# Kernel optimization log

Measured on AMD Instinct MI355X. Metric: run time of the kernel, lower is better.

The kernel has to match this reference:

```python
import jax, jax.numpy as jnp
import numpy as np

B, T, IN, H, Z, DH, K = 512, 256, 5, 256, 128, 512, 20
OUT = 6 * K + 3


def setup_inputs() -> dict:
    key = jax.random.key(0)
    ks = jax.random.split(key, 24)
    p = lambda k, shp: jax.random.normal(k, shp, dtype=jnp.float32) * 0.05
    return {
        "s": jax.random.normal(ks[0], (B, T, IN), dtype=jnp.float32),
        "epsilon": jax.random.normal(ks[1], (Z,), dtype=jnp.float32),
        "Wih_f": p(ks[2], (4 * H, IN)), "Whh_f": p(ks[3], (4 * H, H)),
        "bih_f": p(ks[4], (4 * H,)), "bhh_f": p(ks[5], (4 * H,)),
        "Wih_b": p(ks[6], (4 * H, IN)), "Whh_b": p(ks[7], (4 * H, H)),
        "bih_b": p(ks[8], (4 * H,)), "bhh_b": p(ks[9], (4 * H,)),
        "W_sigma": p(ks[10], (Z, 2 * H)), "b_sigma": p(ks[11], (Z,)),
        "W_mu": p(ks[12], (Z, 2 * H)), "b_mu": p(ks[13], (Z,)),
        "W_h0": p(ks[14], (DH, Z)), "b_h0": p(ks[15], (DH,)),
        "Wih_d": p(ks[16], (4 * DH, IN + Z)), "Whh_d": p(ks[17], (4 * DH, DH)),
        "bih_d": p(ks[18], (4 * DH,)), "bhh_d": p(ks[19], (4 * DH,)),
        "W_dec": p(ks[20], (OUT, DH)), "b_dec": p(ks[21], (OUT,)),
    }


def _lstm_scan(x, Wih, Whh, b, reverse):
    # x: [T, B, in]; PyTorch gate order i, f, g, o
    Hh = Whh.shape[1]
    h0 = jnp.zeros((x.shape[1], Hh), x.dtype)

    def step(carry, xt):
        h, c = carry
        g = xt @ Wih.T + h @ Whh.T + b
        i, f, gg, o = jnp.split(g, 4, axis=-1)
        c = jax.nn.sigmoid(f) * c + jax.nn.sigmoid(i) * jnp.tanh(gg)
        h = jax.nn.sigmoid(o) * jnp.tanh(c)
        return (h, c), h

    _, hs = jax.lax.scan(step, (h0, h0), x, reverse=reverse)
    return hs  # [T, B, Hh]


def _mdn(y):
    # y: [..., 123] -> per-mixture (pi, mu1, mu2, sx, sy, corr) + 3 pen logits
    mix = y[..., :6 * K].reshape(y.shape[:-1] + (K, 6))
    pi = jax.nn.softmax(mix[..., 0], axis=-1)
    out_mix = jnp.stack(
        [pi, mix[..., 1], mix[..., 2], jnp.exp(mix[..., 3]),
         jnp.exp(mix[..., 4]), jnp.tanh(mix[..., 5])], axis=-1)
    pen = jax.nn.softmax(y[..., 6 * K:], axis=-1)
    return jnp.concatenate([out_mix.reshape(y.shape[:-1] + (6 * K,)), pen], axis=-1)


def reference(s, epsilon, Wih_f, Whh_f, bih_f, bhh_f, Wih_b, Whh_b, bih_b, bhh_b,
              W_sigma, b_sigma, W_mu, b_mu, W_h0, b_h0,
              Wih_d, Whh_d, bih_d, bhh_d, W_dec, b_dec):
    x = jnp.transpose(s, (1, 0, 2))  # [T, B, 5]
    hf = _lstm_scan(x, Wih_f, Whh_f, bih_f + bhh_f, False)
    hb = _lstm_scan(x, Wih_b, Whh_b, bih_b + bhh_b, True)
    h = jnp.concatenate([hf[-1], hb[-1]], axis=-1)  # output at last time step, [B, 512]
    presig = h @ W_sigma.T + b_sigma
    mu = h @ W_mu.T + b_mu
    sigma = jnp.exp(presig / 2)
    z = mu + sigma * epsilon  # [B, Z]
    h0 = jnp.tanh(z @ W_h0.T + b_h0)
    c0 = jnp.zeros((s.shape[0], DH), s.dtype)
    s0 = jnp.tile(jnp.array([0.0, 0.0, 1.0, 0.0, 0.0], s.dtype), (s.shape[0], 1))
    dec_in = jnp.concatenate([s0[None], x[:T - 1]], axis=0)  # [T, B, 5]
    bdec = bih_d + bhh_d

    def step(carry, st):
        hh, cc = carry
        xt = jnp.concatenate([st, z], axis=-1)  # [B, 133]
        g = xt @ Wih_d.T + hh @ Whh_d.T + bdec
        i, f, gg, o = jnp.split(g, 4, axis=-1)
        cc = jax.nn.sigmoid(f) * cc + jax.nn.sigmoid(i) * jnp.tanh(gg)
        hh = jax.nn.sigmoid(o) * jnp.tanh(cc)
        y = hh @ W_dec.T + b_dec
        return (hh, cc), y

    _, ys = jax.lax.scan(step, (h0, c0), dec_in)  # [T, B, 123]
    output = _mdn(jnp.transpose(ys, (1, 0, 2)))   # [B, T, 123]
    return (output, mu, presig)
```

## Files before the change

kernel.cpp:

```cpp
#include <hip/hip_runtime.h>

typedef unsigned short u16;
typedef unsigned long long u64;
typedef __attribute__((ext_vector_type(8))) short bfrag;
typedef __attribute__((ext_vector_type(4))) float f32x4;

#define MFMA __builtin_amdgcn_mfma_f32_16x16x32_bf16

#define OFF_FLAGS 0ull
#define OFF_HENC  4096ull
#define OFF_WENC  528384ull
#define OFF_WDEC  1118208ull
#define OFF_WY    3870720ull
#define OFF_WMS   4001792ull
#define OFF_WH0   4280320ull
#define OFF_HDEC  4444160ull
#define OFF_HLAT  5492736ull
#define OFF_AZ    6049792ull
#define OFF_SX    6213632ull

__device__ __forceinline__ u16 f2bf(float f) {
  union { float f; unsigned int i; } v; v.f = f;
  unsigned int r = v.i + 0x7fffu + ((v.i >> 16) & 1u);
  return (u16)(r >> 16);
}
__device__ __forceinline__ float sigm(float x) { return 1.0f / (1.0f + __expf(-x)); }
__device__ __forceinline__ float tanh_(float x) {
  float a = fabsf(x);
  float e = __expf(-2.0f * a);
  float r = (1.0f - e) / (1.0f + e);
  return x < 0.0f ? -r : r;
}

__device__ __forceinline__ u64 aload(const u64* p) {
  return __hip_atomic_load(p, __ATOMIC_RELAXED, __HIP_MEMORY_SCOPE_AGENT);
}
__device__ __forceinline__ void astore(u64* p, u64 v) {
  __hip_atomic_store(p, v, __ATOMIC_RELAXED, __HIP_MEMORY_SCOPE_AGENT);
}
__device__ __forceinline__ float afload(const float* p) {
  return __hip_atomic_load(p, __ATOMIC_RELAXED, __HIP_MEMORY_SCOPE_AGENT);
}
__device__ __forceinline__ void afstore(float* p, float v) {
  __hip_atomic_store(p, v, __ATOMIC_RELAXED, __HIP_MEMORY_SCOPE_AGENT);
}

__device__ __forceinline__ void gwait(int* base, int ep, int tid, int* sdead) {
  if (ep > 0) {
    if (tid < 32 && *sdead == 0) {
      int* fp = base + tid;
      int spin = 0;
      while (__hip_atomic_load(fp, __ATOMIC_RELAXED, __HIP_MEMORY_SCOPE_AGENT) < ep) {
        __builtin_amdgcn_s_sleep(1);
        if (++spin > (1 << 18)) { *sdead = 1; break; }
      }
    }
  }
  __syncthreads();
  asm volatile("" ::: "memory");
}
__device__ __forceinline__ void garrive(int* base, int m, int ep, int tid) {
  asm volatile("s_waitcnt vmcnt(0)" ::: "memory");
  __syncthreads();
  if (tid == 0)
    __hip_atomic_store(base + m, ep, __ATOMIC_RELAXED, __HIP_MEMORY_SCOPE_AGENT);
}

__global__ void pack_wenc(const float* __restrict__ Whh, const float* __restrict__ Wih,
                          const float* __restrict__ bi, const float* __restrict__ bh,
                          u16* __restrict__ out) {
  int idx = blockIdx.x * 256 + threadIdx.x;
  if (idx >= 294912) return;
  int m = idx / 9216, within = idx % 9216;
  int kb = within >> 10, rest = within & 1023;
  int ng = rest >> 9, l = (rest >> 3) & 63, j = rest & 7;
  int nl = ng * 16 + (l & 15);
  int u = nl >> 2, g = nl & 3;
  int row = g * 256 + m * 8 + u;
  int k = kb * 32 + (l >> 4) * 8 + j;
  float v = 0.f;
  if (k < 256) v = Whh[row * 256 + k];
  else if (k < 261) v = Wih[row * 5 + (k - 256)];
  else if (k == 261) v = bi[row] + bh[row];
  out[idx] = f2bf(v);
}

__global__ void pack_wdec(const float* __restrict__ Whh, const float* __restrict__ Wih,
                          const float* __restrict__ bi, const float* __restrict__ bh,
                          u16* __restrict__ out) {
  int idx = blockIdx.x * 256 + threadIdx.x;
  if (idx >= 1376256) return;
  int m = idx / 43008, within = idx % 43008;
  int kb = within >> 11, rest = within & 2047;
  int w = rest >> 9, l = (rest >> 3) & 63, j = rest & 7;
  int nl = w * 16 + (l & 15);
  int u = nl >> 2, g = nl & 3;
  int row = g * 512 + m * 16 + u;
  int k = kb * 32 + (l >> 4) * 8 + j;
  float v = 0.f;
  if (k < 512) v = Whh[row * 512 + k];
  else if (k < 640) v = Wih[row * 133 + 5 + (k - 512)];
  else if (k < 645) v = Wih[row * 133 + (k - 640)];
  else if (k == 645) v = bi[row] + bh[row];
  out[idx] = f2bf(v);
}

__global__ void pack_wy(const float* __restrict__ Wd, u16* __restrict__ out) {
  int idx = blockIdx.x * 256 + threadIdx.x;
  if (idx >= 65536) return;
  int m = idx >> 13, within = idx & 8191;
  int kb = within >> 9, rest = within & 511;
  int l = rest >> 3, j = rest & 7;
  int row = m * 16 + (l & 15);
  int k = kb * 32 + (l >> 4) * 8 + j;
  float v = (row < 123 && k < 512) ? Wd[row * 512 + k] : 0.f;
  out[idx] = f2bf(v);
}

__global__ void pack_wms(const float* __restrict__ Wmu, const float* __restrict__ bmu,
                         const float* __restrict__ Wsig, const float* __restrict__ bsig,
                         u16* __restrict__ out) {
  int idx = blockIdx.x * 256 + threadIdx.x;
  if (idx >= 139264) return;
  int r = idx / 544, k = idx % 544;
  float v = 0.f;
  if (r < 128) {
    if (k < 512) v = Wmu[r * 512 + k];
    else if (k == 512) v = bmu[r];
  } else {
    int r2 = r - 128;
    if (k < 512) v = Wsig[r2 * 512 + k];
    else if (k == 512) v = bsig[r2];
  }
  out[idx] = f2bf(v);
}

__global__ void pack_wh0(const float* __restrict__ Wh0, const float* __restrict__ bh0,
                         u16* __restrict__ out) {
  int idx = blockIdx.x * 256 + threadIdx.x;
  if (idx >= 81920) return;
  int r = idx / 160, k = idx % 160;
  float v = 0.f;
  if (k < 128) v = Wh0[r * 128 + k];
  else if (k == 128) v = bh0[r];
  out[idx] = f2bf(v);
}

__global__ void pack_sx(const float* __restrict__ s, u16* __restrict__ out) {
  int idx = blockIdx.x * 256 + threadIdx.x;
  if (idx >= 1048576) return;
  int j = idx & 7, b = (idx >> 3) & 511, t = idx >> 12;
  u16 v;
  if (j < 5) v = f2bf(s[((size_t)b * 256 + t) * 5 + j]);
  else v = (j == 5) ? (u16)0x3F80 : (u16)0;
  out[idx] = v;
}

__global__ __launch_bounds__(256, 1) void rnn_persist(
    int* __restrict__ flags, u16* __restrict__ henc,
    const u16* __restrict__ WENCP, const u16* __restrict__ WDECP,
    const u16* __restrict__ WYP, const u16* __restrict__ WMSP, const u16* __restrict__ WH0P,
    u16* __restrict__ hdec, u16* __restrict__ hlat, u16* __restrict__ Az,
    const u16* __restrict__ SXD,
    const float* __restrict__ s, const float* __restrict__ eps,
    const float* __restrict__ Wih_b, const float* __restrict__ bih_b,
    const float* __restrict__ bhh_b,
    const float* __restrict__ b_dec, float* __restrict__ out)
{
  __shared__ __align__(16) u16 sm[72960];
  __shared__ __align__(16) float gbuf[2112];
  __shared__ __align__(16) u16 hst[1024];
  __shared__ int sdead;

  const int tid = threadIdx.x;
  const int blk = blockIdx.x;
  const int g = blk & 7;
  const int m = blk >> 3;
  const int B0 = g * 64;
  const int w = tid >> 6, l = tid & 63;
  const int lr = l & 15, ko = (l >> 4) * 8;
  int* FA = flags + g * 128;
  int* FB = FA + 64;

  float* out_mu = out + 16121856;
  float* out_ps = out + 16187392;

  const int gcol = m * 16 + lr;
  float bd = 0.f;
  if (m < 8 && gcol < 123) bd = b_dec[gcol];

  if (tid == 0) sdead = 0;
  {
    bfrag zz = {0, 0, 0, 0, 0, 0, 0, 0};
    #pragma unroll
    for (int i = 0; i < 5; ++i) {
      int c = i * 256 + tid;
      if (c < 1184) *(bfrag*)(sm + c * 8) = zz;
    }
  }
  {
    const u16* src = WENCP + (size_t)m * 9216;
    #pragma unroll
    for (int i = 0; i < 5; ++i) {
      int c = i * 256 + tid;
      if (c < 1152) *(bfrag*)(sm + 21760 + c * 8) = *(const bfrag*)(src + c * 8);
    }
  }
  __syncthreads();

  float c_enc0 = 0.f, c_enc1 = 0.f;
  #pragma unroll 1
  for (int t = 0; t < 256; ++t) {
    #pragma unroll
    for (int X = 0; X < 2; ++X) {
      int* F = X ? FB : FA;
      gwait(F, t, tid, &sdead);
      const u64* hs = (const u64*)(henc + (size_t)((t + 1) & 1) * 131072 +
                                   (size_t)(B0 + X * 32) * 256);
      u64 hv[8];
      #pragma unroll
      for (int i = 0; i < 8; ++i) hv[i] = aload(hs + i * 256 + tid);
      #pragma unroll
      for (int i = 0; i < 8; ++i) {
        int idx = i * 256 + tid;
        *(u64*)(sm + (idx >> 6) * 296 + (idx & 63) * 4) = hv[i];
      }
      if (tid < 64) {
        int row = tid >> 1, q = tid & 1;
        *(u64*)(sm + row * 296 + 256 + q * 4) =
            *(const u64*)(SXD + ((size_t)(t * 512 + B0 + X * 32 + row)) * 8 + q * 4);
      }
      __syncthreads();
      const int mt = w >> 1, ng = w & 1;
      f32x4 acc = {0.f, 0.f, 0.f, 0.f};
      #pragma unroll
      for (int kb = 0; kb < 9; ++kb) {
        bfrag a = *(const bfrag*)(sm + (mt * 16 + lr) * 296 + kb * 32 + ko);
        bfrag bw = *(const bfrag*)(sm + 21760 + (kb * 2 + ng) * 512 + l * 8);
        acc = MFMA(a, bw, acc, 0, 0, 0);
      }
      #pragma unroll
      for (int j = 0; j < 4; ++j)
        gbuf[(mt * 16 + (l >> 4) * 4 + j) * 33 + ng * 16 + lr] = acc[j];
      __syncthreads();
      {
        int bl = tid >> 3, u = tid & 7;
        float gi = gbuf[bl * 33 + u * 4 + 0], gf = gbuf[bl * 33 + u * 4 + 1];
        float gg = gbuf[bl * 33 + u * 4 + 2], go = gbuf[bl * 33 + u * 4 + 3];
        float cprev = (X == 0) ? c_enc0 : c_enc1;
        float c = sigm(gf) * cprev + sigm(gi) * tanh_(gg);
        if (X == 0) c_enc0 = c; else c_enc1 = c;
        hst[bl * 8 + u] = f2bf(sigm(go) * tanh_(c));
      }
      __syncthreads();
      if (tid < 64) {
        int row = tid >> 1, q = tid & 1;
        u64 v = *(const u64*)(hst + row * 8 + q * 4);
        astore((u64*)(henc + (size_t)(t & 1) * 131072 +
                      (size_t)(B0 + X * 32 + row) * 256 + m * 8) + q, v);
      }
      garrive(F, m, t + 1, tid);
    }
  }

  u16* lat_hf = (u16*)gbuf;
  u16* lat_hb = (u16*)gbuf + 512;
  u16* lat_z  = (u16*)gbuf + 1024;

  gwait(FA, 256, tid, &sdead);
  gwait(FB, 256, tid, &sdead);
  {
    const u16* src = WDECP + (size_t)m * 43008;
    #pragma unroll 1
    for (int i = 0; i < 21; ++i) {
      int c = i * 256 + tid;
      *(bfrag*)(sm + 21760 + c * 8) = *(const bfrag*)(src + c * 8);
    }
  }
  if (m < 8) {
    const u16* src = WYP + (size_t)m * 8192;
    #pragma unroll
    for (int i = 0; i < 4; ++i) {
      int c = i * 256 + tid;
      *(bfrag*)(sm + 64768 + c * 8) = *(const bfrag*)(src + c * 8);
    }
  }
  #pragma unroll
  for (int r = 0; r < 2; ++r) {
    int b = B0 + m * 2 + r;
    if (tid < 64) {
      u64 v = aload((const u64*)(henc + 131072 + (size_t)b * 256) + tid);
      *(u64*)(lat_hf + r * 256 + tid * 4) = v;
    }
    {
      const float* xr = s + ((size_t)b * 256 + 255) * 5;
      float x0 = xr[0], x1 = xr[1], x2 = xr[2], x3 = xr[3], x4 = xr[4];
      int n = tid;
      float gv[4];
      #pragma unroll
      for (int gg = 0; gg < 4; ++gg) {
        int row = gg * 256 + n;
        gv[gg] = bih_b[row] + bhh_b[row] + x0 * Wih_b[row * 5] + x1 * Wih_b[row * 5 + 1] +
                 x2 * Wih_b[row * 5 + 2] + x3 * Wih_b[row * 5 + 3] + x4 * Wih_b[row * 5 + 4];
      }
      float c = sigm(gv[0]) * tanh_(gv[2]);
      lat_hb[r * 256 + n] = f2bf(sigm(gv[3]) * tanh_(c));
    }
  }
  __syncthreads();
  #pragma unroll
  for (int it = 0; it < 2; ++it) {
    int idx = it * 256 + tid;
    if (idx < 272) {
      int rr = idx / 136, u = idx % 136;
      u64 pv = 0;
      #pragma unroll
      for (int q = 0; q < 4; ++q) {
        int c = u * 4 + q;
        u16 x;
        if (c < 256) x = lat_hf[rr * 256 + c];
        else if (c < 512) x = lat_hb[rr * 256 + c - 256];
        else if (c == 512) x = 0x3F80;
        else x = 0;
        pv |= ((u64)x) << (q * 16);
      }
      astore((u64*)(hlat + (size_t)(B0 + m * 2 + rr) * 544) + u, pv);
    }
  }
  garrive(FA, m, 257, tid);

  gwait(FA, 257, tid, &sdead);
  {
    const int bH = m >> 4, cT = m & 15;
    const u64* src = (const u64*)(hlat + (size_t)(B0 + bH * 32) * 544);
    u64 sv[17];
    #pragma unroll
    for (int i = 0; i < 17; ++i) sv[i] = aload(src + i * 256 + tid);
    #pragma unroll
    for (int i = 0; i < 17; ++i) *(u64*)(sm + (i * 256 + tid) * 4) = sv[i];
    __syncthreads();
    if (w < 2) {
      f32x4 acc = {0.f, 0.f, 0.f, 0.f};
      const u16* bp = WMSP + (size_t)(cT * 16 + lr) * 544 + ko;
      #pragma unroll
      for (int kb = 0; kb < 17; ++kb) {
        bfrag a = *(const bfrag*)(sm + (w * 16 + lr) * 544 + kb * 32 + ko);
        bfrag bb = *(const bfrag*)(bp + kb * 32);
        acc = MFMA(a, bb, acc, 0, 0, 0);
      }
      int nc = cT * 16 + lr;
      #pragma unroll
      for (int j = 0; j < 4; ++j) {
        int b = B0 + bH * 32 + w * 16 + (l >> 4) * 4 + j;
        if (nc < 128) afstore(out_mu + (size_t)b * 128 + nc, acc[j]);
        else afstore(out_ps + (size_t)b * 128 + nc - 128, acc[j]);
      }
    }
  }
  garrive(FA, m, 258, tid);

  gwait(FA, 258, tid, &sdead);
  {
    int r = tid >> 7, zj = tid & 127;
    int b = B0 + m * 2 + r;
    float mu = afload(out_mu + (size_t)b * 128 + zj);
    float ps = afload(out_ps + (size_t)b * 128 + zj);
    float z = mu + __expf(0.5f * ps) * eps[zj];
    lat_z[r * 128 + zj] = f2bf(z);
  }
  __syncthreads();
  if (tid < 80) {
    int r = tid / 40, u = tid % 40;
    u64 pv = 0;
    #pragma unroll
    for (int q = 0; q < 4; ++q) {
      int c = u * 4 + q;
      u16 x;
      if (c < 128) x = lat_z[r * 128 + c];
      else if (c == 128) x = 0x3F80;
      else x = 0;
      pv |= ((u64)x) << (q * 16);
    }
    astore((u64*)(Az + (size_t)(B0 + m * 2 + r) * 160) + u, pv);
  }
  garrive(FA, m, 259, tid);

  gwait(FA, 259, tid, &sdead);
  u64 zreg0[4], zreg1[4];
  {
    int r = tid >> 3;
    #pragma unroll
    for (int i = 0; i < 4; ++i) {
      int uu = (tid & 7) * 4 + i;
      zreg0[i] = aload((const u64*)(Az + (size_t)(B0 + r) * 160) + uu);
      zreg1[i] = aload((const u64*)(Az + (size_t)(B0 + 32 + r) * 160) + uu);
    }
  }
  {
    const u64* src = (const u64*)(Az + (size_t)B0 * 160);
    u64 sv[10];
    #pragma unroll
    for (int i = 0; i < 10; ++i) sv[i] = aload(src + i * 256 + tid);
    #pragma unroll
    for (int i = 0; i < 10; ++i) *(u64*)(sm + (i * 256 + tid) * 4) = sv[i];
    __syncthreads();
    f32x4 acc = {0.f, 0.f, 0.f, 0.f};
    const u16* bp = WH0P + (size_t)(m * 16 + lr) * 160 + ko;
    #pragma unroll
    for (int kb = 0; kb < 5; ++kb) {
      bfrag a = *(const bfrag*)(sm + (w * 16 + lr) * 160 + kb * 32 + ko);
      bfrag bb = *(const bfrag*)(bp + kb * 32);
      acc = MFMA(a, bb, acc, 0, 0, 0);
    }
    #pragma unroll
    for (int j = 0; j < 4; ++j)
      hst[(w * 16 + (l >> 4) * 4 + j) * 16 + lr] = f2bf(tanh_(acc[j]));
  }
  __syncthreads();
  #pragma unroll
  for (int i = 0; i < 5; ++i) {
    int idx = i * 256 + tid;
    if (idx < 1120) {
      int row = idx / 35, c = idx % 35;
      sm[row * 680 + 645 + c] = (c == 0) ? 0x3F80 : 0;
    }
  }
  {
    int row = tid >> 2, q = tid & 3;
    u64 v = *(const u64*)(hst + row * 16 + q * 4);
    astore((u64*)(hdec + 262144 + (size_t)(B0 + row) * 512 + m * 16) + q, v);
  }
  garrive(FA, m, 260, tid);
  if (tid == 0)
    __hip_atomic_store(FB + m, 257, __ATOMIC_RELAXED, __HIP_MEMORY_SCOPE_AGENT);

  float c_dec00 = 0.f, c_dec01 = 0.f, c_dec10 = 0.f, c_dec11 = 0.f;
  #pragma unroll 1
  for (int t = 0; t < 256; ++t) {
    #pragma unroll
    for (int X = 0; X < 2; ++X) {
      int* F = X ? FB : FA;
      int base = X ? 257 : 260;
      gwait(F, base + t, tid, &sdead);
      const u64* hs = (const u64*)(hdec + (size_t)((t + 1) & 1) * 262144 +
                                   (size_t)(B0 + X * 32) * 512);
      u64 hv[16];
      #pragma unroll
      for (int i = 0; i < 16; ++i) hv[i] = aload(hs + i * 256 + tid);
      #pragma unroll
      for (int i = 0; i < 16; ++i) {
        int idx = i * 256 + tid;
        *(u64*)(sm + (idx >> 7) * 680 + (idx & 127) * 4) = hv[i];
      }
      {
        int r = tid >> 3;
        #pragma unroll
        for (int i = 0; i < 4; ++i) {
          int uu = (tid & 7) * 4 + i;
          *(u64*)(sm + r * 680 + 512 + uu * 4) = (X == 0) ? zreg0[i] : zreg1[i];
        }
      }
      if (tid < 64) {
        int row = tid >> 1, q = tid & 1;
        u64 v;
        if (t == 0) v = q ? 0x000000003F800000ULL : 0x00003F8000000000ULL;
        else v = *(const u64*)(SXD + ((size_t)((t - 1) * 512 + B0 + X * 32 + row)) * 8 + q * 4);
        *(u64*)(sm + row * 680 + 640 + q * 4) = v;
      }
      __syncthreads();
      const int mtd = w & 1, nb = (w >> 1) * 2;
      const bool doy = (m < 8) && (w < 2) && (t > 0);
      f32x4 acc0 = {0.f, 0.f, 0.f, 0.f}, acc1 = {0.f, 0.f, 0.f, 0.f}, accy = {0.f, 0.f, 0.f, 0.f};
      #pragma unroll
      for (int kb = 0; kb < 21; ++kb) {
        bfrag a  = *(const bfrag*)(sm + (mtd * 16 + lr) * 680 + kb * 32 + ko);
        bfrag b0 = *(const bfrag*)(sm + 21760 + kb * 2048 + nb * 512 + l * 8);
        bfrag b1 = *(const bfrag*)(sm + 21760 + kb * 2048 + (nb + 1) * 512 + l * 8);
        acc0 = MFMA(a, b0, acc0, 0, 0, 0);
        acc1 = MFMA(a, b1, acc1, 0, 0, 0);
        if (kb < 16 && doy) {
          bfrag by = *(const bfrag*)(sm + 64768 + kb * 512 + l * 8);
          accy = MFMA(a, by, accy, 0, 0, 0);
        }
      }
      if (doy && gcol < 123) {
        int brow = B0 + X * 32 + w * 16 + (l >> 4) * 4;
        #pragma unroll
        for (int j = 0; j < 4; ++j)
          out[((size_t)(brow + j) * 256 + (t - 1)) * 123 + gcol] = accy[j] + bd;
      }
      #pragma unroll
      for (int j = 0; j < 4; ++j) {
        int grow = mtd * 16 + (l >> 4) * 4 + j;
        gbuf[grow * 66 + nb * 16 + lr] = acc0[j];
        gbuf[grow * 66 + (nb + 1) * 16 + lr] = acc1[j];
      }
      __syncthreads();
      #pragma unroll
      for (int p = 0; p < 2; ++p) {
        int idx = p * 256 + tid;
        int bl = idx >> 4, u = idx & 15;
        float gi = gbuf[bl * 66 + u * 4 + 0], gf = gbuf[bl * 66 + u * 4 + 1];
        float gg = gbuf[bl * 66 + u * 4 + 2], go = gbuf[bl * 66 + u * 4 + 3];
        float cprev = (X == 0) ? (p == 0 ? c_dec00 : c_dec01) : (p == 0 ? c_dec10 : c_dec11);
        float c = sigm(gf) * cprev + sigm(gi) * tanh_(gg);
        if (X == 0) { if (p == 0) c_dec00 = c; else c_dec01 = c; }
        else        { if (p == 0) c_dec10 = c; else c_dec11 = c; }
        hst[bl * 16 + u] = f2bf(sigm(go) * tanh_(c));
      }
      __syncthreads();
      if (tid < 128) {
        int row = tid >> 2, q = tid & 3;
        u64 v = *(const u64*)(hst + row * 16 + q * 4);
        astore((u64*)(hdec + (size_t)(t & 1) * 262144 +
                      (size_t)(B0 + X * 32 + row) * 512 + m * 16) + q, v);
      }
      garrive(F, m, base + t + 1, tid);
    }
  }

  gwait(FA, 516, tid, &sdead);
  gwait(FB, 513, tid, &sdead);
  #pragma unroll
  for (int X = 0; X < 2; ++X) {
    const u64* hsrc = (const u64*)(hdec + 262144 + (size_t)(B0 + X * 32) * 512);
    u64 hv[16];
    #pragma unroll
    for (int i = 0; i < 16; ++i) hv[i] = aload(hsrc + i * 256 + tid);
    #pragma unroll
    for (int i = 0; i < 16; ++i) {
      int idx = i * 256 + tid;
      *(u64*)(sm + (idx >> 7) * 680 + (idx & 127) * 4) = hv[i];
    }
    __syncthreads();
    if (m < 8 && w < 2) {
      f32x4 accy = {0.f, 0.f, 0.f, 0.f};
      #pragma unroll
      for (int kb = 0; kb < 16; ++kb) {
        bfrag a = *(const bfrag*)(sm + (w * 16 + lr) * 680 + kb * 32 + ko);
        bfrag by = *(const bfrag*)(sm + 64768 + kb * 512 + l * 8);
        accy = MFMA(a, by, accy, 0, 0, 0);
      }
      if (gcol < 123) {
        int brow = B0 + X * 32 + w * 16 + (l >> 4) * 4;
        #pragma unroll
        for (int j = 0; j < 4; ++j)
          out[((size_t)(brow + j) * 256 + 255) * 123 + gcol] = accy[j] + bd;
      }
    }
    __syncthreads();
  }
}

__global__ __launch_bounds__(64) void mdn_final(float* __restrict__ out) {
  __shared__ float rows[64 * 123];
  const int tid = threadIdx.x;
  float4* g4 = (float4*)(out + (size_t)blockIdx.x * 64 * 123);
  #pragma unroll
  for (int i = 0; i < 31; ++i) {
    int c = i * 64 + tid;
    if (c < 1968) ((float4*)rows)[c] = g4[c];
  }
  __syncthreads();
  {
    float* r = rows + tid * 123;
    float m1 = -1e30f;
    #pragma unroll
    for (int k = 0; k < 20; ++k) m1 = fmaxf(m1, r[6 * k]);
    float s1 = 0.f;
    #pragma unroll
    for (int k = 0; k < 20; ++k) s1 += __expf(r[6 * k] - m1);
    float i1 = 1.f / s1;
    #pragma unroll
    for (int k = 0; k < 20; ++k) {
      r[6 * k] = __expf(r[6 * k] - m1) * i1;
      r[6 * k + 3] = __expf(r[6 * k + 3]);
      r[6 * k + 4] = __expf(r[6 * k + 4]);
      r[6 * k + 5] = tanh_(r[6 * k + 5]);
    }
    float p0 = r[120], p1 = r[121], p2 = r[122];
    float mp = fmaxf(p0, fmaxf(p1, p2));
    float e0 = __expf(p0 - mp), e1 = __expf(p1 - mp), e2 = __expf(p2 - mp);
    float ip = 1.f / (e0 + e1 + e2);
    r[120] = e0 * ip; r[121] = e1 * ip; r[122] = e2 * ip;
  }
  __syncthreads();
  #pragma unroll
  for (int i = 0; i < 31; ++i) {
    int c = i * 64 + tid;
    if (c < 1968) g4[c] = ((float4*)rows)[c];
  }
}

extern "C" void kernel_launch(void* const* d_in, const int* in_sizes, int n_in,
                              void* d_out, int out_size, void* d_ws, size_t ws_size,
                              hipStream_t stream) {
  const float* s       = (const float*)d_in[0];
  const float* eps     = (const float*)d_in[1];
  const float* Wih_f   = (const float*)d_in[2];
  const float* Whh_f   = (const float*)d_in[3];
  const float* bih_f   = (const float*)d_in[4];
  const float* bhh_f   = (const float*)d_in[5];
  const float* Wih_b   = (const float*)d_in[6];
  const float* bih_b   = (const float*)d_in[8];
  const float* bhh_b   = (const float*)d_in[9];
  const float* W_sigma = (const float*)d_in[10];
  const float* b_sigma = (const float*)d_in[11];
  const float* W_mu    = (const float*)d_in[12];
  const float* b_mu    = (const float*)d_in[13];
  const float* W_h0    = (const float*)d_in[14];
  const float* b_h0    = (const float*)d_in[15];
  const float* Wih_d   = (const float*)d_in[16];
  const float* Whh_d   = (const float*)d_in[17];
  const float* bih_d   = (const float*)d_in[18];
  const float* bhh_d   = (const float*)d_in[19];
  const float* W_dec   = (const float*)d_in[20];
  const float* b_dec   = (const float*)d_in[21];

  char* ws = (char*)d_ws;
  int* FLAGS  = (int*)(ws + OFF_FLAGS);
  u16* HENC   = (u16*)(ws + OFF_HENC);
  u16* WENCP  = (u16*)(ws + OFF_WENC);
  u16* WDECP  = (u16*)(ws + OFF_WDEC);
  u16* WYP    = (u16*)(ws + OFF_WY);
  u16* WMSP   = (u16*)(ws + OFF_WMS);
  u16* WH0P   = (u16*)(ws + OFF_WH0);
  u16* HDEC   = (u16*)(ws + OFF_HDEC);
  u16* HLAT   = (u16*)(ws + OFF_HLAT);
  u16* AZ     = (u16*)(ws + OFF_AZ);
  u16* SXD    = (u16*)(ws + OFF_SX);
  float* out  = (float*)d_out;

  hipMemsetAsync(ws, 0, 4096 + 524288, stream);

  pack_wenc<<<1152, 256, 0, stream>>>(Whh_f, Wih_f, bih_f, bhh_f, WENCP);
  pack_wdec<<<5376, 256, 0, stream>>>(Whh_d, Wih_d, bih_d, bhh_d, WDECP);
  pack_wy<<<256, 256, 0, stream>>>(W_dec, WYP);
  pack_wms<<<544, 256, 0, stream>>>(W_mu, b_mu, W_sigma, b_sigma, WMSP);
  pack_wh0<<<320, 256, 0, stream>>>(W_h0, b_h0, WH0P);
  pack_sx<<<4096, 256, 0, stream>>>(s, SXD);

  rnn_persist<<<256, 256, 0, stream>>>(FLAGS, HENC, WENCP, WDECP, WYP, WMSP, WH0P,
                                       HDEC, HLAT, AZ, SXD, s, eps,
                                       Wih_b, bih_b, bhh_b, b_dec, out);

  mdn_final<<<2048, 64, 0, stream>>>(out);

  (void)in_sizes; (void)n_in; (void)out_size; (void)ws_size;
}
```

Measured before the change: 2.991 ms.

## Prefetch next half-batch hidden state during compute in persistent LSTM loops

The encoder and decoder recurrent loops are flattened into a single 512-iteration loop over (timestep, half-batch). Each iteration polls the flag for the next half-batch and issues its global hidden-state and input loads into registers before the current MFMA and gate work, so the load latency is hidden behind compute. The flag layout is split into separate encoder, decoder and latent-phase counters, which widens the zeroed workspace region. The decoder's constant-1 bias column now comes from the packed input rows rather than a separate LSTM pad. The extra in-flight registers (16 u64 per thread) and the more delicate cross-block ordering add register pressure and some correctness risk.

```diff
diff --git a/kernel.cpp b/kernel.cpp
--- a/kernel.cpp
+++ b/kernel.cpp
@@ -1,23 +1,26 @@
 #include <hip/hip_runtime.h>
 
 typedef unsigned short u16;
+typedef unsigned int u32;
 typedef unsigned long long u64;
 typedef __attribute__((ext_vector_type(8))) short bfrag;
 typedef __attribute__((ext_vector_type(4))) float f32x4;
 
 #define MFMA __builtin_amdgcn_mfma_f32_16x16x32_bf16
+#define VMWAIT0 asm volatile("s_waitcnt vmcnt(0)" ::: "memory")
 
 #define OFF_FLAGS 0ull
-#define OFF_HENC  4096ull
-#define OFF_WENC  528384ull
-#define OFF_WDEC  1118208ull
-#define OFF_WY    3870720ull
-#define OFF_WMS   4001792ull
-#define OFF_WH0   4280320ull
-#define OFF_HDEC  4444160ull
-#define OFF_HLAT  5492736ull
-#define OFF_AZ    6049792ull
-#define OFF_SX    6213632ull
+#define OFF_HENC  10240ull
+#define MEMSET_BYTES 534528ull
+#define OFF_WENC  534528ull
+#define OFF_WDEC  1124352ull
+#define OFF_WY    3876864ull
+#define OFF_WMS   4007936ull
+#define OFF_WH0   4286464ull
+#define OFF_HDEC  4450304ull
+#define OFF_HLAT  5498880ull
+#define OFF_AZ    6055936ull
+#define OFF_SX    6219776ull
 
 __device__ __forceinline__ u16 f2bf(float f) {
   union { float f; unsigned int i; } v; v.f = f;
@@ -45,25 +48,27 @@
   __hip_atomic_store(p, v, __ATOMIC_RELAXED, __HIP_MEMORY_SCOPE_AGENT);
 }
 
+__device__ __forceinline__ void fpoll(int* F, int need, int tid, int* sdead) {
+  if (need > 0 && tid < 32 && *sdead == 0) {
+    int spin = 0;
+    while (__hip_atomic_load(F + tid, __ATOMIC_RELAXED, __HIP_MEMORY_SCOPE_AGENT) < need) {
+      __builtin_amdgcn_s_sleep(1);
+      if (++spin > (1 << 18)) { *sdead = 1; break; }
+    }
+  }
+  asm volatile("" ::: "memory");
+}
+__device__ __forceinline__ void fset(int* F, int m, int v) {
+  __hip_atomic_store(F + m, v, __ATOMIC_RELAXED, __HIP_MEMORY_SCOPE_AGENT);
+}
 __device__ __forceinline__ void gwait(int* base, int ep, int tid, int* sdead) {
-  if (ep > 0) {
-    if (tid < 32 && *sdead == 0) {
-      int* fp = base + tid;
-      int spin = 0;
-      while (__hip_atomic_load(fp, __ATOMIC_RELAXED, __HIP_MEMORY_SCOPE_AGENT) < ep) {
-        __builtin_amdgcn_s_sleep(1);
-        if (++spin > (1 << 18)) { *sdead = 1; break; }
-      }
-    }
-  }
-  __syncthreads();
-  asm volatile("" ::: "memory");
+  fpoll(base, ep, tid, sdead);
+  __syncthreads();
 }
 __device__ __forceinline__ void garrive(int* base, int m, int ep, int tid) {
-  asm volatile("s_waitcnt vmcnt(0)" ::: "memory");
-  __syncthreads();
-  if (tid == 0)
-    __hip_atomic_store(base + m, ep, __ATOMIC_RELAXED, __HIP_MEMORY_SCOPE_AGENT);
+  VMWAIT0;
+  __syncthreads();
+  if (tid == 0) fset(base, m, ep);
 }
 
 __global__ void pack_wenc(const float* __restrict__ Whh, const float* __restrict__ Wih,
@@ -157,11 +162,10 @@
 }
 
 __global__ __launch_bounds__(256, 1) void rnn_persist(
-    int* __restrict__ flags, u16* __restrict__ henc,
+    int* __restrict__ flags, u16* __restrict__ henc, u16* __restrict__ hdec,
     const u16* __restrict__ WENCP, const u16* __restrict__ WDECP,
     const u16* __restrict__ WYP, const u16* __restrict__ WMSP, const u16* __restrict__ WH0P,
-    u16* __restrict__ hdec, u16* __restrict__ hlat, u16* __restrict__ Az,
-    const u16* __restrict__ SXD,
+    u16* __restrict__ hlat, u16* __restrict__ Az, const u16* __restrict__ SXD,
     const float* __restrict__ s, const float* __restrict__ eps,
     const float* __restrict__ Wih_b, const float* __restrict__ bih_b,
     const float* __restrict__ bhh_b,
@@ -179,8 +183,11 @@
   const int B0 = g * 64;
   const int w = tid >> 6, l = tid & 63;
   const int lr = l & 15, ko = (l >> 4) * 8;
-  int* FA = flags + g * 128;
-  int* FB = FA + 64;
+  int* FE0 = flags + g * 320;
+  int* FE1 = FE0 + 64;
+  int* FD0 = FE0 + 128;
+  int* FD1 = FE0 + 192;
+  int* FL  = FE0 + 256;
 
   float* out_mu = out + 16121856;
   float* out_ps = out + 16187392;
@@ -208,67 +215,81 @@
   }
   __syncthreads();
 
+  u64 hv[16];
+  u64 sxv = 0;
+
+  {
+    const u64* hs = (const u64*)(henc + 131072 + (size_t)B0 * 256);
+    #pragma unroll
+    for (int i = 0; i < 8; ++i) hv[i] = aload(hs + i * 256 + tid);
+    if (tid < 64)
+      sxv = *(const u64*)(SXD + (size_t)(B0 + (tid >> 1)) * 8 + (tid & 1) * 4);
+  }
   float c_enc0 = 0.f, c_enc1 = 0.f;
   #pragma unroll 1
-  for (int t = 0; t < 256; ++t) {
-    #pragma unroll
-    for (int X = 0; X < 2; ++X) {
-      int* F = X ? FB : FA;
-      gwait(F, t, tid, &sdead);
-      const u64* hs = (const u64*)(henc + (size_t)((t + 1) & 1) * 131072 +
-                                   (size_t)(B0 + X * 32) * 256);
-      u64 hv[8];
+  for (int e = 0; e < 512; ++e) {
+    const int X = e & 1, t = e >> 1;
+    VMWAIT0;
+    #pragma unroll
+    for (int i = 0; i < 8; ++i) {
+      int idx = i * 256 + tid;
+      *(u64*)(sm + (idx >> 6) * 296 + (idx & 63) * 4) = hv[i];
+    }
+    if (tid < 64) *(u64*)(sm + (tid >> 1) * 296 + 256 + (tid & 1) * 4) = sxv;
+    if (e < 511) {
+      int Xn = (e + 1) & 1, tn = (e + 1) >> 1;
+      fpoll(Xn ? FE1 : FE0, tn, tid, &sdead);
+    }
+    __syncthreads();
+    if (e < 511) {
+      int Xn = (e + 1) & 1, tn = (e + 1) >> 1;
+      const u64* hs = (const u64*)(henc + (size_t)((tn + 1) & 1) * 131072 +
+                                   (size_t)(B0 + Xn * 32) * 256);
       #pragma unroll
       for (int i = 0; i < 8; ++i) hv[i] = aload(hs + i * 256 + tid);
-      #pragma unroll
-      for (int i = 0; i < 8; ++i) {
-        int idx = i * 256 + tid;
-        *(u64*)(sm + (idx >> 6) * 296 + (idx & 63) * 4) = hv[i];
-      }
-      if (tid < 64) {
-        int row = tid >> 1, q = tid & 1;
-        *(u64*)(sm + row * 296 + 256 + q * 4) =
-            *(const u64*)(SXD + ((size_t)(t * 512 + B0 + X * 32 + row)) * 8 + q * 4);
-      }
-      __syncthreads();
-      const int mt = w >> 1, ng = w & 1;
-      f32x4 acc = {0.f, 0.f, 0.f, 0.f};
-      #pragma unroll
-      for (int kb = 0; kb < 9; ++kb) {
-        bfrag a = *(const bfrag*)(sm + (mt * 16 + lr) * 296 + kb * 32 + ko);
-        bfrag bw = *(const bfrag*)(sm + 21760 + (kb * 2 + ng) * 512 + l * 8);
-        acc = MFMA(a, bw, acc, 0, 0, 0);
-      }
-      #pragma unroll
-      for (int j = 0; j < 4; ++j)
-        gbuf[(mt * 16 + (l >> 4) * 4 + j) * 33 + ng * 16 + lr] = acc[j];
-      __syncthreads();
-      {
-        int bl = tid >> 3, u = tid & 7;
-        float gi = gbuf[bl * 33 + u * 4 + 0], gf = gbuf[bl * 33 + u * 4 + 1];
-        float gg = gbuf[bl * 33 + u * 4 + 2], go = gbuf[bl * 33 + u * 4 + 3];
-        float cprev = (X == 0) ? c_enc0 : c_enc1;
-        float c = sigm(gf) * cprev + sigm(gi) * tanh_(gg);
-        if (X == 0) c_enc0 = c; else c_enc1 = c;
-        hst[bl * 8 + u] = f2bf(sigm(go) * tanh_(c));
-      }
-      __syncthreads();
-      if (tid < 64) {
-        int row = tid >> 1, q = tid & 1;
-        u64 v = *(const u64*)(hst + row * 8 + q * 4);
-        astore((u64*)(henc + (size_t)(t & 1) * 131072 +
-                      (size_t)(B0 + X * 32 + row) * 256 + m * 8) + q, v);
-      }
-      garrive(F, m, t + 1, tid);
-    }
+      if (tid < 64)
+        sxv = *(const u64*)(SXD + (size_t)(tn * 512 + B0 + Xn * 32 + (tid >> 1)) * 8 + (tid & 1) * 4);
+    }
+    const int mt = w >> 1, ng = w & 1;
+    f32x4 acc = {0.f, 0.f, 0.f, 0.f};
+    #pragma unroll
+    for (int kb = 0; kb < 9; ++kb) {
+      bfrag a = *(const bfrag*)(sm + (mt * 16 + lr) * 296 + kb * 32 + ko);
+      bfrag bw = *(const bfrag*)(sm + 21760 + (kb * 2 + ng) * 512 + l * 8);
+      acc = MFMA(a, bw, acc, 0, 0, 0);
+    }
+    #pragma unroll
+    for (int j = 0; j < 4; ++j)
+      gbuf[(mt * 16 + (l >> 4) * 4 + j) * 33 + ng * 16 + lr] = acc[j];
+    __syncthreads();
+    {
+      int bl = tid >> 3, u = tid & 7;
+      float gi = gbuf[bl * 33 + u * 4 + 0], gf = gbuf[bl * 33 + u * 4 + 1];
+      float gg = gbuf[bl * 33 + u * 4 + 2], go = gbuf[bl * 33 + u * 4 + 3];
+      float cprev = (X == 0) ? c_enc0 : c_enc1;
+      float c = sigm(gf) * cprev + sigm(gi) * tanh_(gg);
+      if (X == 0) c_enc0 = c; else c_enc1 = c;
+      hst[bl * 8 + u] = f2bf(sigm(go) * tanh_(c));
+    }
+    __syncthreads();
+    if (tid < 64) {
+      int row = tid >> 1, q = tid & 1;
+      u64 v = *(const u64*)(hst + row * 8 + q * 4);
+      astore((u64*)(henc + (size_t)(t & 1) * 131072 +
+                    (size_t)(B0 + X * 32 + row) * 256 + m * 8) + q, v);
+    }
+    VMWAIT0;
+    __syncthreads();
+    if (tid == 0) fset(X ? FE1 : FE0, m, t + 1);
   }
 
   u16* lat_hf = (u16*)gbuf;
   u16* lat_hb = (u16*)gbuf + 512;
   u16* lat_z  = (u16*)gbuf + 1024;
 
-  gwait(FA, 256, tid, &sdead);
-  gwait(FB, 256, tid, &sdead);
+  fpoll(FE0, 256, tid, &sdead);
+  fpoll(FE1, 256, tid, &sdead);
+  __syncthreads();
   {
     const u16* src = WDECP + (size_t)m * 43008;
     #pragma unroll 1
@@ -327,9 +348,8 @@
       astore((u64*)(hlat + (size_t)(B0 + m * 2 + rr) * 544) + u, pv);
     }
   }
-  garrive(FA, m, 257, tid);
-
-  gwait(FA, 257, tid, &sdead);
+  garrive(FL, m, 1, tid);
+  gwait(FL, 1, tid, &sdead);
   {
     const int bH = m >> 4, cT = m & 15;
     const u64* src = (const u64*)(hlat + (size_t)(B0 + bH * 32) * 544);
@@ -357,9 +377,8 @@
       }
     }
   }
-  garrive(FA, m, 258, tid);
-
-  gwait(FA, 258, tid, &sdead);
+  garrive(FL, m, 2, tid);
+  gwait(FL, 2, tid, &sdead);
   {
     int r = tid >> 7, zj = tid & 127;
     int b = B0 + m * 2 + r;
@@ -383,9 +402,8 @@
     }
     astore((u64*)(Az + (size_t)(B0 + m * 2 + r) * 160) + u, pv);
   }
-  garrive(FA, m, 259, tid);
-
-  gwait(FA, 259, tid, &sdead);
+  garrive(FL, m, 3, tid);
+  gwait(FL, 3, tid, &sdead);
   u64 zreg0[4], zreg1[4];
   {
     int r = tid >> 3;
@@ -418,11 +436,11 @@
   }
   __syncthreads();
   #pragma unroll
-  for (int i = 0; i < 5; ++i) {
+  for (int i = 0; i < 4; ++i) {
     int idx = i * 256 + tid;
-    if (idx < 1120) {
-      int row = idx / 35, c = idx % 35;
-      sm[row * 680 + 645 + c] = (c == 0) ? 0x3F80 : 0;
+    if (idx < 1024) {
+      int row = idx >> 5, c = idx & 31;
+      sm[row * 680 + 648 + c] = 0;
     }
   }
   {
@@ -430,103 +448,111 @@
     u64 v = *(const u64*)(hst + row * 16 + q * 4);
     astore((u64*)(hdec + 262144 + (size_t)(B0 + row) * 512 + m * 16) + q, v);
   }
-  garrive(FA, m, 260, tid);
-  if (tid == 0)
-    __hip_atomic_store(FB + m, 257, __ATOMIC_RELAXED, __HIP_MEMORY_SCOPE_AGENT);
-
-  float c_dec00 = 0.f, c_dec01 = 0.f, c_dec10 = 0.f, c_dec11 = 0.f;
+  garrive(FL, m, 4, tid);
+  gwait(FL, 4, tid, &sdead);
+
+  {
+    const u64* hs = (const u64*)(hdec + 262144 + (size_t)B0 * 512);
+    #pragma unroll
+    for (int i = 0; i < 16; ++i) hv[i] = aload(hs + i * 256 + tid);
+  }
+  float c00 = 0.f, c01 = 0.f, c10 = 0.f, c11 = 0.f;
   #pragma unroll 1
-  for (int t = 0; t < 256; ++t) {
-    #pragma unroll
-    for (int X = 0; X < 2; ++X) {
-      int* F = X ? FB : FA;
-      int base = X ? 257 : 260;
-      gwait(F, base + t, tid, &sdead);
-      const u64* hs = (const u64*)(hdec + (size_t)((t + 1) & 1) * 262144 +
-                                   (size_t)(B0 + X * 32) * 512);
-      u64 hv[16];
+  for (int e = 0; e < 512; ++e) {
+    const int X = e & 1, t = e >> 1;
+    VMWAIT0;
+    #pragma unroll
+    for (int i = 0; i < 16; ++i) {
+      int idx = i * 256 + tid;
+      *(u64*)(sm + (idx >> 7) * 680 + (idx & 127) * 4) = hv[i];
+    }
+    {
+      int r = tid >> 3;
+      #pragma unroll
+      for (int i = 0; i < 4; ++i) {
+        int uu = (tid & 7) * 4 + i;
+        *(u64*)(sm + r * 680 + 512 + uu * 4) = (X == 0) ? zreg0[i] : zreg1[i];
+      }
+    }
+    if (tid < 64) {
+      u64 v = sxv;
+      if (t == 0) v = (tid & 1) ? 0x000000003F800000ULL : 0x00003F8000000000ULL;
+      *(u64*)(sm + (tid >> 1) * 680 + 640 + (tid & 1) * 4) = v;
+    }
+    if (e < 511) {
+      int Xn = (e + 1) & 1, tn = (e + 1) >> 1;
+      fpoll(Xn ? FD1 : FD0, tn, tid, &sdead);
+    }
+    __syncthreads();
+    if (e < 511) {
+      int Xn = (e + 1) & 1, tn = (e + 1) >> 1;
+      const u64* hs = (const u64*)(hdec + (size_t)((tn + 1) & 1) * 262144 +
+                                   (size_t)(B0 + Xn * 32) * 512);
       #pragma unroll
       for (int i = 0; i < 16; ++i) hv[i] = aload(hs + i * 256 + tid);
-      #pragma unroll
-      for (int i = 0; i < 16; ++i) {
-        int idx = i * 256 + tid;
-        *(u64*)(sm + (idx >> 7) * 680 + (idx & 127) * 4) = hv[i];
-      }
-      {
-        int r = tid >> 3;
-        #pragma unroll
-        for (int i = 0; i < 4; ++i) {
-          int uu = (tid & 7) * 4 + i;
-          *(u64*)(sm + r * 680 + 512 + uu * 4) = (X == 0) ? zreg0[i] : zreg1[i];
-        }
-      }
-      if (tid < 64) {
-        int row = tid >> 1, q = tid & 1;
-        u64 v;
-        if (t == 0) v = q ? 0x000000003F800000ULL : 0x00003F8000000000ULL;
-        else v = *(const u64*)(SXD + ((size_t)((t - 1) * 512 + B0 + X * 32 + row)) * 8 + q * 4);
-        *(u64*)(sm + row * 680 + 640 + q * 4) = v;
-      }
-      __syncthreads();
-      const int mtd = w & 1, nb = (w >> 1) * 2;
-      const bool doy = (m < 8) && (w < 2) && (t > 0);
-      f32x4 acc0 = {0.f, 0.f, 0.f, 0.f}, acc1 = {0.f, 0.f, 0.f, 0.f}, accy = {0.f, 0.f, 0.f, 0.f};
-      #pragma unroll
-      for (int kb = 0; kb < 21; ++kb) {
-        bfrag a  = *(const bfrag*)(sm + (mtd * 16 + lr) * 680 + kb * 32 + ko);
-        bfrag b0 = *(const bfrag*)(sm + 21760 + kb * 2048 + nb * 512 + l * 8);
-        bfrag b1 = *(const bfrag*)(sm + 21760 + kb * 2048 + (nb + 1) * 512 + l * 8);
-        acc0 = MFMA(a, b0, acc0, 0, 0, 0);
-        acc1 = MFMA(a, b1, acc1, 0, 0, 0);
-        if (kb < 16 && doy) {
-          bfrag by = *(const bfrag*)(sm + 64768 + kb * 512 + l * 8);
-          accy = MFMA(a, by, accy, 0, 0, 0);
-        }
-      }
-      if (doy && gcol < 123) {
-        int brow = B0 + X * 32 + w * 16 + (l >> 4) * 4;
-        #pragma unroll
-        for (int j = 0; j < 4; ++j)
-          out[((size_t)(brow + j) * 256 + (t - 1)) * 123 + gcol] = accy[j] + bd;
-      }
-      #pragma unroll
-      for (int j = 0; j < 4; ++j) {
-        int grow = mtd * 16 + (l >> 4) * 4 + j;
-        gbuf[grow * 66 + nb * 16 + lr] = acc0[j];
-        gbuf[grow * 66 + (nb + 1) * 16 + lr] = acc1[j];
-      }
-      __syncthreads();
-      #pragma unroll
-      for (int p = 0; p < 2; ++p) {
-        int idx = p * 256 + tid;
-        int bl = idx >> 4, u = idx & 15;
-        float gi = gbuf[bl * 66 + u * 4 + 0], gf = gbuf[bl * 66 + u * 4 + 1];
-        float gg = gbuf[bl * 66 + u * 4 + 2], go = gbuf[bl * 66 + u * 4 + 3];
-        float cprev = (X == 0) ? (p == 0 ? c_dec00 : c_dec01) : (p == 0 ? c_dec10 : c_dec11);
-        float c = sigm(gf) * cprev + sigm(gi) * tanh_(gg);
-        if (X == 0) { if (p == 0) c_dec00 = c; else c_dec01 = c; }
-        else        { if (p == 0) c_dec10 = c; else c_dec11 = c; }
-        hst[bl * 16 + u] = f2bf(sigm(go) * tanh_(c));
-      }
-      __syncthreads();
-      if (tid < 128) {
-        int row = tid >> 2, q = tid & 3;
-        u64 v = *(const u64*)(hst + row * 16 + q * 4);
-        astore((u64*)(hdec + (size_t)(t & 1) * 262144 +
-                      (size_t)(B0 + X * 32 + row) * 512 + m * 16) + q, v);
-      }
-      garrive(F, m, base + t + 1, tid);
-    }
-  }
-
-  gwait(FA, 516, tid, &sdead);
-  gwait(FB, 513, tid, &sdead);
-  #pragma unroll
-  for (int X = 0; X < 2; ++X) {
-    const u64* hsrc = (const u64*)(hdec + 262144 + (size_t)(B0 + X * 32) * 512);
-    u64 hv[16];
-    #pragma unroll
-    for (int i = 0; i < 16; ++i) hv[i] = aload(hsrc + i * 256 + tid);
+      if (tid < 64 && tn >= 1)
+        sxv = *(const u64*)(SXD + (size_t)((tn - 1) * 512 + B0 + Xn * 32 + (tid >> 1)) * 8 + (tid & 1) * 4);
+    }
+    const int mtd = w & 1, nb = (w >> 1) * 2;
+    const bool doy = (m < 8) && (w < 2) && (t > 0);
+    f32x4 acc0 = {0.f, 0.f, 0.f, 0.f}, acc1 = {0.f, 0.f, 0.f, 0.f}, accy = {0.f, 0.f, 0.f, 0.f};
+    #pragma unroll
+    for (int kb = 0; kb < 21; ++kb) {
+      bfrag a  = *(const bfrag*)(sm + (mtd * 16 + lr) * 680 + kb * 32 + ko);
+      bfrag b0 = *(const bfrag*)(sm + 21760 + kb * 2048 + nb * 512 + l * 8);
+      bfrag b1 = *(const bfrag*)(sm + 21760 + kb * 2048 + (nb + 1) * 512 + l * 8);
+      acc0 = MFMA(a, b0, acc0, 0, 0, 0);
+      acc1 = MFMA(a, b1, acc1, 0, 0, 0);
+      if (kb < 16 && doy) {
+        bfrag by = *(const bfrag*)(sm + 64768 + kb * 512 + l * 8);
+        accy = MFMA(a, by, accy, 0, 0, 0);
+      }
+    }
+    if (doy && gcol < 123) {
+      int brow = B0 + X * 32 + w * 16 + (l >> 4) * 4;
+      #pragma unroll
+      for (int j = 0; j < 4; ++j)
+        out[((size_t)(brow + j) * 256 + (t - 1)) * 123 + gcol] = accy[j] + bd;
+    }
+    #pragma unroll
+    for (int j = 0; j < 4; ++j) {
+      int grow = mtd * 16 + (l >> 4) * 4 + j;
+      gbuf[grow * 66 + nb * 16 + lr] = acc0[j];
+      gbuf[grow * 66 + (nb + 1) * 16 + lr] = acc1[j];
+    }
+    __syncthreads();
+    #pragma unroll
+    for (int p = 0; p < 2; ++p) {
+      int idx = p * 256 + tid;
+      int bl = idx >> 4, u = idx & 15;
+      float gi = gbuf[bl * 66 + u * 4 + 0], gf = gbuf[bl * 66 + u * 4 + 1];
+      float gg = gbuf[bl * 66 + u * 4 + 2], go = gbuf[bl * 66 + u * 4 + 3];
+      float cprev = (X == 0) ? (p == 0 ? c00 : c01) : (p == 0 ? c10 : c11);
+      float c = sigm(gf) * cprev + sigm(gi) * tanh_(gg);
+      if (X == 0) { if (p == 0) c00 = c; else c01 = c; }
+      else        { if (p == 0) c10 = c; else c11 = c; }
+      hst[bl * 16 + u] = f2bf(sigm(go) * tanh_(c));
+    }
+    __syncthreads();
+    if (tid < 128) {
+      int row = tid >> 2, q = tid & 3;
+      u64 v = *(const u64*)(hst + row * 16 + q * 4);
+      astore((u64*)(hdec + (size_t)(t & 1) * 262144 +
+                    (size_t)(B0 + X * 32 + row) * 512 + m * 16) + q, v);
+    }
+    VMWAIT0;
+    __syncthreads();
+    if (tid == 0) fset(X ? FD1 : FD0, m, t + 1);
+  }
+
+  fpoll(FD0, 256, tid, &sdead);
+  fpoll(FD1, 256, tid, &sdead);
+  __syncthreads();
+  #pragma unroll 1
+  for (int hh = 0; hh < 2; ++hh) {
+    const u64* hs = (const u64*)(hdec + 262144 + (size_t)(B0 + hh * 32) * 512);
+    #pragma unroll
+    for (int i = 0; i < 16; ++i) hv[i] = aload(hs + i * 256 + tid);
     #pragma unroll
     for (int i = 0; i < 16; ++i) {
       int idx = i * 256 + tid;
@@ -542,7 +568,7 @@
         accy = MFMA(a, by, accy, 0, 0, 0);
       }
       if (gcol < 123) {
-        int brow = B0 + X * 32 + w * 16 + (l >> 4) * 4;
+        int brow = B0 + hh * 32 + w * 16 + (l >> 4) * 4;
         #pragma unroll
         for (int j = 0; j < 4; ++j)
           out[((size_t)(brow + j) * 256 + 255) * 123 + gcol] = accy[j] + bd;
@@ -631,7 +657,7 @@
   u16* SXD    = (u16*)(ws + OFF_SX);
   float* out  = (float*)d_out;
 
-  hipMemsetAsync(ws, 0, 4096 + 524288, stream);
+  hipMemsetAsync(ws, 0, (size_t)MEMSET_BYTES, stream);
 
   pack_wenc<<<1152, 256, 0, stream>>>(Whh_f, Wih_f, bih_f, bhh_f, WENCP);
   pack_wdec<<<5376, 256, 0, stream>>>(Whh_d, Wih_d, bih_d, bhh_d, WDECP);
@@ -640,8 +666,8 @@
   pack_wh0<<<320, 256, 0, stream>>>(W_h0, b_h0, WH0P);
   pack_sx<<<4096, 256, 0, stream>>>(s, SXD);
 
-  rnn_persist<<<256, 256, 0, stream>>>(FLAGS, HENC, WENCP, WDECP, WYP, WMSP, WH0P,
-                                       HDEC, HLAT, AZ, SXD, s, eps,
+  rnn_persist<<<256, 256, 0, stream>>>(FLAGS, HENC, HDEC, WENCP, WDECP, WYP, WMSP, WH0P,
+                                       HLAT, AZ, SXD, s, eps,
                                        Wih_b, bih_b, bhh_b, b_dec, out);
 
   mdn_final<<<2048, 64, 0, stream>>>(out);
```

New measurement: 2.997 ms. Within noise of the previous version (+0.2%).
